# Performance work log

Measured on AMD Instinct MI355X. Metric: run time of the kernel, lower is better.

The kernel has to match this reference:

```python
import jax, jax.numpy as jnp
import numpy as np

N_NODES = 100000
N_EDGES = 1600000
IN_CH = 64
HID = 128
N_CLASSES = 10
N_GRAPHS = 64


def setup_inputs() -> dict:
    key = jax.random.key(0)
    ks = jax.random.split(key, 10)
    x = jax.random.normal(ks[0], (N_NODES, IN_CH), dtype=jnp.float32)
    edge_index = jax.random.randint(ks[1], (2, N_EDGES), 0, N_NODES, dtype=jnp.int64)
    batch = jnp.sort(jax.random.randint(ks[2], (N_NODES,), 0, N_GRAPHS, dtype=jnp.int64))
    # GCNConv / Linear parameters (glorot-ish scaling)
    W1 = jax.random.normal(ks[3], (IN_CH, HID), dtype=jnp.float32) * (1.0 / np.sqrt(IN_CH))
    b1 = jnp.zeros((HID,), dtype=jnp.float32)
    W2 = jax.random.normal(ks[4], (HID, HID), dtype=jnp.float32) * (1.0 / np.sqrt(HID))
    b2 = jnp.zeros((HID,), dtype=jnp.float32)
    Wc = jax.random.normal(ks[5], (HID, N_CLASSES), dtype=jnp.float32) * (1.0 / np.sqrt(HID))
    bc = jnp.zeros((N_CLASSES,), dtype=jnp.float32)
    return {"x": x, "W1": W1, "b1": b1, "W2": W2, "b2": b2,
            "Wc": Wc, "bc": bc, "edge_index": edge_index, "batch": batch}


def reference(x, W1, b1, W2, b2, Wc, bc, edge_index, batch):
    N = x.shape[0]
    # add self-loops (PyG GCNConv default)
    loop = jnp.arange(N, dtype=edge_index.dtype)
    src = jnp.concatenate([edge_index[0], loop])  # message sources (j)
    dst = jnp.concatenate([edge_index[1], loop])  # aggregation targets (i)
    # symmetric normalization D^{-1/2} (A+I) D^{-1/2}
    deg = jax.ops.segment_sum(jnp.ones_like(dst, dtype=x.dtype), dst, num_segments=N)
    dinv = jnp.where(deg > 0, jax.lax.rsqrt(jnp.maximum(deg, 1e-12)), 0.0)
    norm = dinv[src] * dinv[dst]  # [E+N]

    def gcn_conv(h, W, b):
        h = h @ W  # transform first, then aggregate (gather-scale-scatter)
        msg = h[src] * norm[:, None]
        return jax.ops.segment_sum(msg, dst, num_segments=N) + b

    h = jax.nn.relu(gcn_conv(x, W1, b1))
    h = jax.nn.relu(gcn_conv(h, W2, b2))
    # global mean pool over graphs
    cnt = jax.ops.segment_sum(jnp.ones((N,), x.dtype), batch, num_segments=N_GRAPHS)
    pooled = jax.ops.segment_sum(h, batch, num_segments=N_GRAPHS) / jnp.maximum(cnt, 1.0)[:, None]
    return pooled @ Wc + bc
```

## Files before the change

kernel.cpp:

```cpp
#include <hip/hip_runtime.h>

#define NN 100000
#define NE 1600000

#define BSHIFT 9
#define NBKT 256
#define BCAP 12288
#define TILE 4096

using half8 = __attribute__((ext_vector_type(8))) _Float16;
using f32x4 = __attribute__((ext_vector_type(4))) float;

__device__ inline unsigned short f2bf(float f) {
    unsigned int u = __float_as_uint(f);
    unsigned int r = (u + 0x7fffu + ((u >> 16) & 1u)) >> 16;
    return (unsigned short)r;
}
__device__ inline float bf2f(unsigned short h) {
    return __uint_as_float(((unsigned int)h) << 16);
}
__device__ inline float bflo(unsigned int v) { return __uint_as_float(v << 16); }
__device__ inline float bfhi(unsigned int v) { return __uint_as_float(v & 0xffff0000u); }
__device__ inline unsigned short f2h(float f) {
    union { _Float16 h; unsigned short u; } c; c.h = (_Float16)f; return c.u;
}

__global__ __launch_bounds__(256) void k_bucket(
    const int* __restrict__ src, const int* __restrict__ dst,
    int* __restrict__ gcnt, unsigned* __restrict__ stage, int E) {
    __shared__ unsigned st[TILE];
    __shared__ unsigned char stb[TILE];
    __shared__ int hist4[4 * NBKT];
    __shared__ int hist[NBKT];
    __shared__ int s[NBKT];
    __shared__ int offs[NBKT];
    __shared__ int cursor[NBKT];
    __shared__ int gbase[NBKT];
    int tid = threadIdx.x;
    int wv = tid >> 6;
    int t0 = blockIdx.x * TILE;
    int m = E - t0; if (m > TILE) m = TILE;

    for (int i = tid; i < 4 * NBKT; i += 256) hist4[i] = 0;
    __syncthreads();
    for (int i = tid; i < m; i += 256)
        atomicAdd(&hist4[wv * NBKT + (dst[t0 + i] >> BSHIFT)], 1);
    __syncthreads();
    int h = hist4[tid] + hist4[NBKT + tid] + hist4[2 * NBKT + tid] + hist4[3 * NBKT + tid];
    hist[tid] = h;
    s[tid] = h;
    __syncthreads();
    for (int off = 1; off < NBKT; off <<= 1) {
        int t = (tid >= off) ? s[tid - off] : 0;
        __syncthreads();
        s[tid] += t;
        __syncthreads();
    }
    offs[tid] = s[tid] - hist[tid];
    cursor[tid] = s[tid] - hist[tid];
    gbase[tid] = atomicAdd(&gcnt[tid], hist[tid]);
    __syncthreads();
    for (int i = tid; i < m; i += 256) {
        int d = dst[t0 + i];
        int b = d >> BSHIFT;
        unsigned packed = ((unsigned)src[t0 + i] << BSHIFT) | (unsigned)(d & 511);
        int pos = atomicAdd(&cursor[b], 1);
        st[pos] = packed;
        stb[pos] = (unsigned char)b;
    }
    __syncthreads();
    for (int i = tid; i < m; i += 256) {
        int b = stb[i];
        int idx = gbase[b] + (i - offs[b]);
        if (idx < BCAP) stage[(size_t)b * BCAP + idx] = st[i];
    }
}

__global__ __launch_bounds__(512) void k_cnt_bucket(
    const unsigned* __restrict__ stage, const int* __restrict__ gcnt,
    int* __restrict__ cnt, int N) {
    __shared__ int h[512];
    int b = blockIdx.x;
    int tid = threadIdx.x;
    h[tid] = 0;
    __syncthreads();
    int n = gcnt[b]; if (n > BCAP) n = BCAP;
    const unsigned* sg = stage + (size_t)b * BCAP;
    for (int i = tid; i < n; i += 512)
        atomicAdd(&h[sg[i] & 511], 1);
    __syncthreads();
    int d = (b << BSHIFT) | tid;
    if (d < N) cnt[d] = h[tid];
}

__global__ void k_dinv(const int* __restrict__ cnt, float* __restrict__ dinv, int N) {
    int i = blockIdx.x * blockDim.x + threadIdx.x;
    if (i < N) dinv[i] = rsqrtf((float)(cnt[i] + 1));
}

__global__ void k_scan1(const int* __restrict__ cnt, int* __restrict__ excl,
                        int* __restrict__ bsums, int N) {
    __shared__ int s[512];
    int tid = threadIdx.x;
    int i = blockIdx.x * 512 + tid;
    int v = (i < N) ? cnt[i] : 0;
    s[tid] = v;
    __syncthreads();
    for (int off = 1; off < 512; off <<= 1) {
        int t = (tid >= off) ? s[tid - off] : 0;
        __syncthreads();
        s[tid] += t;
        __syncthreads();
    }
    if (i < N) excl[i] = s[tid] - v;
    if (tid == 511) bsums[blockIdx.x] = s[511];
}

__global__ void k_scan2(int* __restrict__ bsums, int nb) {
    if (blockIdx.x == 0 && threadIdx.x == 0) {
        int run = 0;
        for (int b = 0; b < nb; ++b) { int t = bsums[b]; bsums[b] = run; run += t; }
    }
}

__global__ void k_scan3(int* __restrict__ row_ptr, const int* __restrict__ bsums,
                        int N, int E) {
    int i = blockIdx.x * blockDim.x + threadIdx.x;
    if (i < N) row_ptr[i] += bsums[i >> 9];
    if (i == 0) row_ptr[N] = E;
}

__global__ __launch_bounds__(512) void k_scatter(
    const unsigned* __restrict__ stage, const int* __restrict__ gcnt,
    const int* __restrict__ row_ptr, int* __restrict__ col, int N) {
    __shared__ int cur[512];
    int b = blockIdx.x;
    int tid = threadIdx.x;
    int d0 = (b << BSHIFT) | tid;
    cur[tid] = (d0 < N) ? row_ptr[d0] : 0;
    __syncthreads();
    int n = gcnt[b]; if (n > BCAP) n = BCAP;
    const unsigned* sg = stage + (size_t)b * BCAP;
    for (int i = tid; i < n; i += 512) {
        unsigned e = sg[i];
        int pos = atomicAdd(&cur[e & 511], 1);
        col[pos] = (int)(e >> BSHIFT);
    }
}


__global__ void k_tobf16(const float* __restrict__ in, unsigned short* __restrict__ out, int n8) {
    int i = blockIdx.x * blockDim.x + threadIdx.x;
    if (i >= n8) return;
    const float4* p = (const float4*)(in + (size_t)i * 8);
    float4 a = p[0], b = p[1];
    uint4 o;
    o.x = (unsigned)f2bf(a.x) | ((unsigned)f2bf(a.y) << 16);
    o.y = (unsigned)f2bf(a.z) | ((unsigned)f2bf(a.w) << 16);
    o.z = (unsigned)f2bf(b.x) | ((unsigned)f2bf(b.y) << 16);
    o.w = (unsigned)f2bf(b.z) | ((unsigned)f2bf(b.w) << 16);
    ((uint4*)out)[i] = o;
}

__global__ void k_packW(const float* __restrict__ W, half8* __restrict__ wpack, int K) {
    int t = blockIdx.x * blockDim.x + threadIdx.x;
    int total = (K / 32) * 8 * 64;
    if (t >= total) return;
    int s = t >> 9;
    int j = (t >> 6) & 7;
    int l = t & 63;
    half8 hv;
#pragma unroll
    for (int jj = 0; jj < 8; ++jj)
        hv[jj] = (_Float16)W[(size_t)(32 * s + 8 * (l >> 4) + jj) * 128 + 16 * j + (l & 15)];
    wpack[t] = hv;
}


template <int C>
__global__ void k_agg(const unsigned short* __restrict__ xb, const int* __restrict__ row_ptr,
                      const int* __restrict__ col, const float* __restrict__ dinv,
                      unsigned short* __restrict__ out, int N) {
    int node = blockIdx.x * (blockDim.x >> 6) + (threadIdx.x >> 6);
    int lane = threadIdx.x & 63;
    if (node >= N) return;
    int beg = row_ptr[node], end = row_ptr[node + 1];
    float di = dinv[node];

    if constexpr (C == 64) {
        float acc = 0.f;
        for (int base = beg; base < end; base += 64) {
            int m = end - base; if (m > 64) m = 64;
            int sel = (lane < m) ? lane : (m - 1);
            int cl = col[base + sel];
            float wl = (lane < m) ? dinv[cl] : 0.f;
            for (int k = 0; k < m; k += 8) {
                int c0 = __shfl(cl, k),     c1 = __shfl(cl, k + 1);
                int c2 = __shfl(cl, k + 2), c3 = __shfl(cl, k + 3);
                int c4 = __shfl(cl, k + 4), c5 = __shfl(cl, k + 5);
                int c6 = __shfl(cl, k + 6), c7 = __shfl(cl, k + 7);
                float w0 = __shfl(wl, k),     w1 = __shfl(wl, k + 1);
                float w2 = __shfl(wl, k + 2), w3 = __shfl(wl, k + 3);
                float w4 = __shfl(wl, k + 4), w5 = __shfl(wl, k + 5);
                float w6 = __shfl(wl, k + 6), w7 = __shfl(wl, k + 7);
                unsigned short v0 = xb[(size_t)c0 * 64 + lane];
                unsigned short v1 = xb[(size_t)c1 * 64 + lane];
                unsigned short v2 = xb[(size_t)c2 * 64 + lane];
                unsigned short v3 = xb[(size_t)c3 * 64 + lane];
                unsigned short v4 = xb[(size_t)c4 * 64 + lane];
                unsigned short v5 = xb[(size_t)c5 * 64 + lane];
                unsigned short v6 = xb[(size_t)c6 * 64 + lane];
                unsigned short v7 = xb[(size_t)c7 * 64 + lane];
                acc += w0 * bf2f(v0) + w1 * bf2f(v1) + w2 * bf2f(v2) + w3 * bf2f(v3)
                     + w4 * bf2f(v4) + w5 * bf2f(v5) + w6 * bf2f(v6) + w7 * bf2f(v7);
            }
        }
        acc = di * acc + di * di * bf2f(xb[(size_t)node * 64 + lane]);
        out[(size_t)node * 64 + lane] = f2h(acc);
    } else {
        const unsigned int* xb2 = (const unsigned int*)xb;
        float ax = 0.f, ay = 0.f;
        for (int base = beg; base < end; base += 64) {
            int m = end - base; if (m > 64) m = 64;
            int sel = (lane < m) ? lane : (m - 1);
            int cl = col[base + sel];
            float wl = (lane < m) ? dinv[cl] : 0.f;
            for (int k = 0; k < m; k += 8) {
                int c0 = __shfl(cl, k),     c1 = __shfl(cl, k + 1);
                int c2 = __shfl(cl, k + 2), c3 = __shfl(cl, k + 3);
                int c4 = __shfl(cl, k + 4), c5 = __shfl(cl, k + 5);
                int c6 = __shfl(cl, k + 6), c7 = __shfl(cl, k + 7);
                float w0 = __shfl(wl, k),     w1 = __shfl(wl, k + 1);
                float w2 = __shfl(wl, k + 2), w3 = __shfl(wl, k + 3);
                float w4 = __shfl(wl, k + 4), w5 = __shfl(wl, k + 5);
                float w6 = __shfl(wl, k + 6), w7 = __shfl(wl, k + 7);
                unsigned int v0 = xb2[(size_t)c0 * 64 + lane];
                unsigned int v1 = xb2[(size_t)c1 * 64 + lane];
                unsigned int v2 = xb2[(size_t)c2 * 64 + lane];
                unsigned int v3 = xb2[(size_t)c3 * 64 + lane];
                unsigned int v4 = xb2[(size_t)c4 * 64 + lane];
                unsigned int v5 = xb2[(size_t)c5 * 64 + lane];
                unsigned int v6 = xb2[(size_t)c6 * 64 + lane];
                unsigned int v7 = xb2[(size_t)c7 * 64 + lane];
                ax += w0 * bflo(v0) + w1 * bflo(v1) + w2 * bflo(v2) + w3 * bflo(v3)
                    + w4 * bflo(v4) + w5 * bflo(v5) + w6 * bflo(v6) + w7 * bflo(v7);
                ay += w0 * bfhi(v0) + w1 * bfhi(v1) + w2 * bfhi(v2) + w3 * bfhi(v3)
                    + w4 * bfhi(v4) + w5 * bfhi(v5) + w6 * bfhi(v6) + w7 * bfhi(v7);
            }
        }
        unsigned int v = xb2[(size_t)node * 64 + lane];
        ax = di * ax + di * di * bflo(v);
        ay = di * ay + di * di * bfhi(v);
        ((unsigned int*)out)[(size_t)node * 64 + lane] =
            (unsigned int)f2h(ax) | ((unsigned int)f2h(ay) << 16);
    }
}


template <int K, bool OUTBF>
__global__ __launch_bounds__(256) void k_gemm_mfma(
    const unsigned short* __restrict__ A, const half8* __restrict__ wpack,
    const float* __restrict__ bias, void* __restrict__ outp, int N) {
    int lane = threadIdx.x & 63;
    int wave = threadIdx.x >> 6;
    int row0 = blockIdx.x * 64 + wave * 16;
    int ar = row0 + (lane & 15);
    if (ar >= N) ar = N - 1;
    const _Float16* Ah = (const _Float16*)A;

    f32x4 acc[8];
#pragma unroll
    for (int j = 0; j < 8; ++j) acc[j] = (f32x4)(0.f);

#pragma unroll
    for (int s = 0; s < K / 32; ++s) {
        half8 av = *(const half8*)(Ah + (size_t)ar * K + 32 * s + 8 * (lane >> 4));
#pragma unroll
        for (int j = 0; j < 8; ++j) {
            half8 bv = wpack[(s * 8 + j) * 64 + lane];
            acc[j] = __builtin_amdgcn_mfma_f32_16x16x32_f16(av, bv, acc[j], 0, 0, 0);
        }
    }

    int rowb = row0 + (lane >> 4) * 4;
#pragma unroll
    for (int j = 0; j < 8; ++j) {
        int colc = j * 16 + (lane & 15);
        float b = bias[colc];
#pragma unroll
        for (int r = 0; r < 4; ++r) {
            int rr = rowb + r;
            if (rr < N) {
                float v = fmaxf(acc[j][r] + b, 0.f);
                if constexpr (OUTBF)
                    ((unsigned short*)outp)[(size_t)rr * 128 + colc] = f2bf(v);
                else
                    ((float*)outp)[(size_t)rr * 128 + colc] = v;
            }
        }
    }
}


__global__ void k_cntg_bs(const int* __restrict__ batch, int* __restrict__ cntg, int N) {
    int g = threadIdx.x;
    if (g >= 64) return;
    int lo = 0, hi = N;
    while (lo < hi) { int mid = (lo + hi) >> 1; if (batch[mid] < g) lo = mid + 1; else hi = mid; }
    int start = lo;
    lo = 0; hi = N;
    while (lo < hi) { int mid = (lo + hi) >> 1; if (batch[mid] < g + 1) lo = mid + 1; else hi = mid; }
    cntg[g] = lo - start;
}

#define POOL_NPB 64
__global__ void k_pool(const float* __restrict__ h, const int* __restrict__ batch,
                       float* __restrict__ pooled, int N) {
    int tid = threadIdx.x;
    int start = blockIdx.x * POOL_NPB;
    int end = start + POOL_NPB;
    if (end > N) end = N;
    if (start >= end) return;
    int curg = batch[start];
    float acc = 0.f;
    for (int n = start; n < end; ++n) {
        int g = batch[n];
        if (g != curg) {
            atomicAdd(&pooled[curg * 128 + tid], acc);
            acc = 0.f;
            curg = g;
        }
        acc += h[(size_t)n * 128 + tid];
    }
    atomicAdd(&pooled[curg * 128 + tid], acc);
}

__global__ void k_final(const float* __restrict__ pooled, const int* __restrict__ cntg,
                        const float* __restrict__ Wc, const float* __restrict__ bc,
                        float* __restrict__ out) {
    for (int idx = threadIdx.x; idx < 64 * 10; idx += 256) {
        int g = idx / 10, c = idx % 10;
        float s = 0.f;
        for (int k = 0; k < 128; ++k) s += pooled[g * 128 + k] * Wc[k * 10 + c];
        float cnt = (float)cntg[g];
        if (cnt < 1.f) cnt = 1.f;
        out[idx] = s / cnt + bc[c];
    }
}


extern "C" void kernel_launch(void* const* d_in, const int* in_sizes, int n_in,
                              void* d_out, int out_size, void* d_ws, size_t ws_size,
                              hipStream_t stream) {
    const float* x  = (const float*)d_in[0];
    const float* W1 = (const float*)d_in[1];
    const float* b1 = (const float*)d_in[2];
    const float* W2 = (const float*)d_in[3];
    const float* b2 = (const float*)d_in[4];
    const float* Wc = (const float*)d_in[5];
    const float* bc = (const float*)d_in[6];
    const int* ei   = (const int*)d_in[7];
    const int* batch = (const int*)d_in[8];

    const int E = in_sizes[7] / 2;
    const int N = in_sizes[8];
    const int* src = ei;
    const int* dst = ei + E;

    char* p = (char*)d_ws;
    auto alloc = [&](size_t bytes) -> void* {
        void* r = (void*)p;
        p += (bytes + 255) & ~(size_t)255;
        return r;
    };
    int*   cnt      = (int*)alloc((size_t)N * 4);
    float* dinv     = (float*)alloc((size_t)N * 4);
    int*   row_ptr  = (int*)alloc((size_t)(N + 1) * 4);
    int*   bsums    = (int*)alloc(4096);
    int*   col      = (int*)alloc((size_t)E * 4);
    int*   gcnt     = (int*)alloc(NBKT * 4);
    unsigned* stage = (unsigned*)alloc((size_t)NBKT * BCAP * 4);
    unsigned short* xb    = (unsigned short*)alloc((size_t)N * 64 * 2);
    unsigned short* h1b   = (unsigned short*)alloc((size_t)N * 128 * 2);
    unsigned short* aggb1 = (unsigned short*)alloc((size_t)N * 64 * 2);
    unsigned short* aggb2 = (unsigned short*)alloc((size_t)N * 128 * 2);
    half8* w1p      = (half8*)alloc(1024 * 16);
    half8* w2p      = (half8*)alloc(2048 * 16);
    float* bufB     = (float*)alloc((size_t)N * 128 * 4);
    float* pooled   = (float*)alloc(64 * 128 * 4);
    int*   cntg     = (int*)alloc(64 * 4);

    hipMemsetAsync(gcnt, 0, NBKT * 4, stream);
    hipMemsetAsync(pooled, 0, 64 * 128 * 4, stream);

    int nb = (N + 511) / 512;

    k_bucket<<<(E + TILE - 1) / TILE, 256, 0, stream>>>(src, dst, gcnt, stage, E);
    k_cnt_bucket<<<nb, 512, 0, stream>>>(stage, gcnt, cnt, N);
    k_dinv<<<(N + 255) / 256, 256, 0, stream>>>(cnt, dinv, N);
    k_scan1<<<nb, 512, 0, stream>>>(cnt, row_ptr, bsums, N);
    k_scan2<<<1, 64, 0, stream>>>(bsums, nb);
    k_scan3<<<(N + 255) / 256, 256, 0, stream>>>(row_ptr, bsums, N, E);
    k_scatter<<<nb, 512, 0, stream>>>(stage, gcnt, row_ptr, col, N);

    k_packW<<<4, 256, 0, stream>>>(W1, w1p, 64);
    k_packW<<<8, 256, 0, stream>>>(W2, w2p, 128);
    k_tobf16<<<(N * 64 / 8 + 255) / 256, 256, 0, stream>>>(x, xb, N * 64 / 8);

    k_agg<64><<<(N + 3) / 4, 256, 0, stream>>>(xb, row_ptr, col, dinv, aggb1, N);
    k_gemm_mfma<64, true><<<(N + 63) / 64, 256, 0, stream>>>(aggb1, w1p, b1, h1b, N);

    k_agg<128><<<(N + 3) / 4, 256, 0, stream>>>(h1b, row_ptr, col, dinv, aggb2, N);
    k_gemm_mfma<128, false><<<(N + 63) / 64, 256, 0, stream>>>(aggb2, w2p, b2, bufB, N);

    k_cntg_bs<<<1, 64, 0, stream>>>(batch, cntg, N);
    k_pool<<<(N + POOL_NPB - 1) / POOL_NPB, 128, 0, stream>>>(bufB, batch, pooled, N);
    k_final<<<1, 256, 0, stream>>>(pooled, cntg, Wc, bc, (float*)d_out);
}
```

Measured before the change: 277.5 us.

## Pre-scale features by source dinv to drop per-edge dinv gathers in aggregation

Folds the source-side D^{-1/2} factor into the features before aggregation: x is scaled by dinv during bf16 conversion, and the layer-1 GEMM epilogue scales its output by dinv. The aggregation kernels then sum raw neighbor rows and apply only the destination dinv, removing the per-edge dinv[col] gather and weight shuffles. It also fuses the dinv computation into the bucket-count kernel, dropping one launch, and stores the layer-2 output as bf16 instead of fp32 to halve pooling traffic. The trade-off is extra bf16 rounding from pre-scaling and from the bf16 final hidden state.

```diff
diff --git a/kernel.cpp b/kernel.cpp
--- a/kernel.cpp
+++ b/kernel.cpp
@@ -78,7 +78,7 @@
 
 __global__ __launch_bounds__(512) void k_cnt_bucket(
     const unsigned* __restrict__ stage, const int* __restrict__ gcnt,
-    int* __restrict__ cnt, int N) {
+    int* __restrict__ cnt, float* __restrict__ dinv, int N) {
     __shared__ int h[512];
     int b = blockIdx.x;
     int tid = threadIdx.x;
@@ -90,12 +90,10 @@
         atomicAdd(&h[sg[i] & 511], 1);
     __syncthreads();
     int d = (b << BSHIFT) | tid;
-    if (d < N) cnt[d] = h[tid];
-}
-
-__global__ void k_dinv(const int* __restrict__ cnt, float* __restrict__ dinv, int N) {
-    int i = blockIdx.x * blockDim.x + threadIdx.x;
-    if (i < N) dinv[i] = rsqrtf((float)(cnt[i] + 1));
+    if (d < N) {
+        cnt[d] = h[tid];
+        dinv[d] = rsqrtf((float)(h[tid] + 1));
+    }
 }
 
 __global__ void k_scan1(const int* __restrict__ cnt, int* __restrict__ excl,
@@ -148,17 +146,18 @@
     }
 }
 
-
-__global__ void k_tobf16(const float* __restrict__ in, unsigned short* __restrict__ out, int n8) {
+__global__ void k_toscaled(const float* __restrict__ in, const float* __restrict__ dinv,
+                           unsigned short* __restrict__ out, int n8) {
     int i = blockIdx.x * blockDim.x + threadIdx.x;
     if (i >= n8) return;
+    float di = dinv[i >> 3];
     const float4* p = (const float4*)(in + (size_t)i * 8);
     float4 a = p[0], b = p[1];
     uint4 o;
-    o.x = (unsigned)f2bf(a.x) | ((unsigned)f2bf(a.y) << 16);
-    o.y = (unsigned)f2bf(a.z) | ((unsigned)f2bf(a.w) << 16);
-    o.z = (unsigned)f2bf(b.x) | ((unsigned)f2bf(b.y) << 16);
-    o.w = (unsigned)f2bf(b.z) | ((unsigned)f2bf(b.w) << 16);
+    o.x = (unsigned)f2bf(di * a.x) | ((unsigned)f2bf(di * a.y) << 16);
+    o.y = (unsigned)f2bf(di * a.z) | ((unsigned)f2bf(di * a.w) << 16);
+    o.z = (unsigned)f2bf(di * b.x) | ((unsigned)f2bf(di * b.y) << 16);
+    o.w = (unsigned)f2bf(di * b.z) | ((unsigned)f2bf(di * b.w) << 16);
     ((uint4*)out)[i] = o;
 }
 
@@ -188,21 +187,17 @@
     float di = dinv[node];
 
     if constexpr (C == 64) {
-        float acc = 0.f;
+        float acc = bf2f(xb[(size_t)node * 64 + lane]);
         for (int base = beg; base < end; base += 64) {
             int m = end - base; if (m > 64) m = 64;
             int sel = (lane < m) ? lane : (m - 1);
             int cl = col[base + sel];
-            float wl = (lane < m) ? dinv[cl] : 0.f;
-            for (int k = 0; k < m; k += 8) {
+            int k = 0;
+            for (; k + 8 <= m; k += 8) {
                 int c0 = __shfl(cl, k),     c1 = __shfl(cl, k + 1);
                 int c2 = __shfl(cl, k + 2), c3 = __shfl(cl, k + 3);
                 int c4 = __shfl(cl, k + 4), c5 = __shfl(cl, k + 5);
                 int c6 = __shfl(cl, k + 6), c7 = __shfl(cl, k + 7);
-                float w0 = __shfl(wl, k),     w1 = __shfl(wl, k + 1);
-                float w2 = __shfl(wl, k + 2), w3 = __shfl(wl, k + 3);
-                float w4 = __shfl(wl, k + 4), w5 = __shfl(wl, k + 5);
-                float w6 = __shfl(wl, k + 6), w7 = __shfl(wl, k + 7);
                 unsigned short v0 = xb[(size_t)c0 * 64 + lane];
                 unsigned short v1 = xb[(size_t)c1 * 64 + lane];
                 unsigned short v2 = xb[(size_t)c2 * 64 + lane];
@@ -211,29 +206,29 @@
                 unsigned short v5 = xb[(size_t)c5 * 64 + lane];
                 unsigned short v6 = xb[(size_t)c6 * 64 + lane];
                 unsigned short v7 = xb[(size_t)c7 * 64 + lane];
-                acc += w0 * bf2f(v0) + w1 * bf2f(v1) + w2 * bf2f(v2) + w3 * bf2f(v3)
-                     + w4 * bf2f(v4) + w5 * bf2f(v5) + w6 * bf2f(v6) + w7 * bf2f(v7);
+                acc += bf2f(v0) + bf2f(v1) + bf2f(v2) + bf2f(v3)
+                     + bf2f(v4) + bf2f(v5) + bf2f(v6) + bf2f(v7);
+            }
+            for (; k < m; ++k) {
+                int c = __shfl(cl, k);
+                acc += bf2f(xb[(size_t)c * 64 + lane]);
             }
         }
-        acc = di * acc + di * di * bf2f(xb[(size_t)node * 64 + lane]);
-        out[(size_t)node * 64 + lane] = f2h(acc);
+        out[(size_t)node * 64 + lane] = f2h(di * acc);
     } else {
         const unsigned int* xb2 = (const unsigned int*)xb;
-        float ax = 0.f, ay = 0.f;
+        unsigned int sv = xb2[(size_t)node * 64 + lane];
+        float ax = bflo(sv), ay = bfhi(sv);
         for (int base = beg; base < end; base += 64) {
             int m = end - base; if (m > 64) m = 64;
             int sel = (lane < m) ? lane : (m - 1);
             int cl = col[base + sel];
-            float wl = (lane < m) ? dinv[cl] : 0.f;
-            for (int k = 0; k < m; k += 8) {
+            int k = 0;
+            for (; k + 8 <= m; k += 8) {
                 int c0 = __shfl(cl, k),     c1 = __shfl(cl, k + 1);
                 int c2 = __shfl(cl, k + 2), c3 = __shfl(cl, k + 3);
                 int c4 = __shfl(cl, k + 4), c5 = __shfl(cl, k + 5);
                 int c6 = __shfl(cl, k + 6), c7 = __shfl(cl, k + 7);
-                float w0 = __shfl(wl, k),     w1 = __shfl(wl, k + 1);
-                float w2 = __shfl(wl, k + 2), w3 = __shfl(wl, k + 3);
-                float w4 = __shfl(wl, k + 4), w5 = __shfl(wl, k + 5);
-                float w6 = __shfl(wl, k + 6), w7 = __shfl(wl, k + 7);
                 unsigned int v0 = xb2[(size_t)c0 * 64 + lane];
                 unsigned int v1 = xb2[(size_t)c1 * 64 + lane];
                 unsigned int v2 = xb2[(size_t)c2 * 64 + lane];
@@ -242,25 +237,29 @@
                 unsigned int v5 = xb2[(size_t)c5 * 64 + lane];
                 unsigned int v6 = xb2[(size_t)c6 * 64 + lane];
                 unsigned int v7 = xb2[(size_t)c7 * 64 + lane];
-                ax += w0 * bflo(v0) + w1 * bflo(v1) + w2 * bflo(v2) + w3 * bflo(v3)
-                    + w4 * bflo(v4) + w5 * bflo(v5) + w6 * bflo(v6) + w7 * bflo(v7);
-                ay += w0 * bfhi(v0) + w1 * bfhi(v1) + w2 * bfhi(v2) + w3 * bfhi(v3)
-                    + w4 * bfhi(v4) + w5 * bfhi(v5) + w6 * bfhi(v6) + w7 * bfhi(v7);
+                ax += bflo(v0) + bflo(v1) + bflo(v2) + bflo(v3)
+                    + bflo(v4) + bflo(v5) + bflo(v6) + bflo(v7);
+                ay += bfhi(v0) + bfhi(v1) + bfhi(v2) + bfhi(v3)
+                    + bfhi(v4) + bfhi(v5) + bfhi(v6) + bfhi(v7);
+            }
+            for (; k < m; ++k) {
+                int c = __shfl(cl, k);
+                unsigned int v = xb2[(size_t)c * 64 + lane];
+                ax += bflo(v);
+                ay += bfhi(v);
             }
         }
-        unsigned int v = xb2[(size_t)node * 64 + lane];
-        ax = di * ax + di * di * bflo(v);
-        ay = di * ay + di * di * bfhi(v);
         ((unsigned int*)out)[(size_t)node * 64 + lane] =
-            (unsigned int)f2h(ax) | ((unsigned int)f2h(ay) << 16);
-    }
-}
-
-
-template <int K, bool OUTBF>
+            (unsigned int)f2h(di * ax) | ((unsigned int)f2h(di * ay) << 16);
+    }
+}
+
+
+template <int K, bool SCALE>
 __global__ __launch_bounds__(256) void k_gemm_mfma(
     const unsigned short* __restrict__ A, const half8* __restrict__ wpack,
-    const float* __restrict__ bias, void* __restrict__ outp, int N) {
+    const float* __restrict__ bias, const float* __restrict__ dinv,
+    unsigned short* __restrict__ outp, int N) {
     int lane = threadIdx.x & 63;
     int wave = threadIdx.x >> 6;
     int row0 = blockIdx.x * 64 + wave * 16;
@@ -283,6 +282,12 @@
     }
 
     int rowb = row0 + (lane >> 4) * 4;
+    float dv[4];
+#pragma unroll
+    for (int r = 0; r < 4; ++r) {
+        int rr = rowb + r; if (rr >= N) rr = N - 1;
+        dv[r] = SCALE ? dinv[rr] : 1.f;
+    }
 #pragma unroll
     for (int j = 0; j < 8; ++j) {
         int colc = j * 16 + (lane & 15);
@@ -292,10 +297,8 @@
             int rr = rowb + r;
             if (rr < N) {
                 float v = fmaxf(acc[j][r] + b, 0.f);
-                if constexpr (OUTBF)
-                    ((unsigned short*)outp)[(size_t)rr * 128 + colc] = f2bf(v);
-                else
-                    ((float*)outp)[(size_t)rr * 128 + colc] = v;
+                if constexpr (SCALE) v *= dv[r];
+                outp[(size_t)rr * 128 + colc] = f2bf(v);
             }
         }
     }
@@ -314,7 +317,7 @@
 }
 
 #define POOL_NPB 64
-__global__ void k_pool(const float* __restrict__ h, const int* __restrict__ batch,
+__global__ void k_pool(const unsigned short* __restrict__ h, const int* __restrict__ batch,
                        float* __restrict__ pooled, int N) {
     int tid = threadIdx.x;
     int start = blockIdx.x * POOL_NPB;
@@ -330,7 +333,7 @@
             acc = 0.f;
             curg = g;
         }
-        acc += h[(size_t)n * 128 + tid];
+        acc += bf2f(h[(size_t)n * 128 + tid]);
     }
     atomicAdd(&pooled[curg * 128 + tid], acc);
 }
@@ -384,9 +387,9 @@
     unsigned short* h1b   = (unsigned short*)alloc((size_t)N * 128 * 2);
     unsigned short* aggb1 = (unsigned short*)alloc((size_t)N * 64 * 2);
     unsigned short* aggb2 = (unsigned short*)alloc((size_t)N * 128 * 2);
+    unsigned short* h2b   = (unsigned short*)alloc((size_t)N * 128 * 2);
     half8* w1p      = (half8*)alloc(1024 * 16);
     half8* w2p      = (half8*)alloc(2048 * 16);
-    float* bufB     = (float*)alloc((size_t)N * 128 * 4);
     float* pooled   = (float*)alloc(64 * 128 * 4);
     int*   cntg     = (int*)alloc(64 * 4);
 
@@ -396,8 +399,7 @@
     int nb = (N + 511) / 512;
 
     k_bucket<<<(E + TILE - 1) / TILE, 256, 0, stream>>>(src, dst, gcnt, stage, E);
-    k_cnt_bucket<<<nb, 512, 0, stream>>>(stage, gcnt, cnt, N);
-    k_dinv<<<(N + 255) / 256, 256, 0, stream>>>(cnt, dinv, N);
+    k_cnt_bucket<<<nb, 512, 0, stream>>>(stage, gcnt, cnt, dinv, N);
     k_scan1<<<nb, 512, 0, stream>>>(cnt, row_ptr, bsums, N);
     k_scan2<<<1, 64, 0, stream>>>(bsums, nb);
     k_scan3<<<(N + 255) / 256, 256, 0, stream>>>(row_ptr, bsums, N, E);
@@ -405,15 +407,15 @@
 
     k_packW<<<4, 256, 0, stream>>>(W1, w1p, 64);
     k_packW<<<8, 256, 0, stream>>>(W2, w2p, 128);
-    k_tobf16<<<(N * 64 / 8 + 255) / 256, 256, 0, stream>>>(x, xb, N * 64 / 8);
+    k_toscaled<<<(N * 8 + 255) / 256, 256, 0, stream>>>(x, dinv, xb, N * 8);
 
     k_agg<64><<<(N + 3) / 4, 256, 0, stream>>>(xb, row_ptr, col, dinv, aggb1, N);
-    k_gemm_mfma<64, true><<<(N + 63) / 64, 256, 0, stream>>>(aggb1, w1p, b1, h1b, N);
+    k_gemm_mfma<64, true><<<(N + 63) / 64, 256, 0, stream>>>(aggb1, w1p, b1, dinv, h1b, N);
 
     k_agg<128><<<(N + 3) / 4, 256, 0, stream>>>(h1b, row_ptr, col, dinv, aggb2, N);
-    k_gemm_mfma<128, false><<<(N + 63) / 64, 256, 0, stream>>>(aggb2, w2p, b2, bufB, N);
+    k_gemm_mfma<128, false><<<(N + 63) / 64, 256, 0, stream>>>(aggb2, w2p, b2, nullptr, h2b, N);
 
     k_cntg_bs<<<1, 64, 0, stream>>>(batch, cntg, N);
-    k_pool<<<(N + POOL_NPB - 1) / POOL_NPB, 128, 0, stream>>>(bufB, batch, pooled, N);
+    k_pool<<<(N + POOL_NPB - 1) / POOL_NPB, 128, 0, stream>>>(h2b, batch, pooled, N);
     k_final<<<1, 256, 0, stream>>>(pooled, cntg, Wc, bc, (float*)d_out);
 }
```

Result: no change. 279.4 us (+0.7%).
